# Kernel optimization log

Hardware: AMD Instinct MI355X
Metric: run time of the kernel (lower is better)

Reference implementation:

```python
import jax, jax.numpy as jnp
import numpy as np

B, S, H, L = 64, 512, 1024, 5  # batch, seq_len, BiLSTM feature dim (2*512), num fine P labels


def setup_inputs() -> dict:
    key = jax.random.key(0)
    ks = jax.random.split(key, 8)
    feats = jax.random.normal(ks[0], (B, S, H), dtype=jnp.float32)
    labels = jax.random.randint(ks[1], (B, S), 0, L)
    mask = jnp.ones((B, S), dtype=bool)  # CRF requires mask[:, 0] all on
    W_tag = jax.random.normal(ks[2], (H, L), dtype=jnp.float32) * 0.02
    b_tag = jnp.zeros((L,), dtype=jnp.float32)
    start_trans = jax.random.normal(ks[3], (L,), dtype=jnp.float32) * 0.1
    end_trans = jax.random.normal(ks[4], (L,), dtype=jnp.float32) * 0.1
    trans = jax.random.normal(ks[5], (L, L), dtype=jnp.float32) * 0.1
    weights = jax.random.uniform(ks[6], (L,), dtype=jnp.float32, minval=0.5, maxval=1.5)
    return dict(feats=feats, labels=labels, mask=mask, W_tag=W_tag, b_tag=b_tag,
                start_trans=start_trans, end_trans=end_trans, trans=trans, weights=weights)


def reference(feats, labels, mask, W_tag, b_tag, start_trans, end_trans, trans, weights):
    # hidden2tag + relu (as in the torch module: probablity = F.relu(self.hidden2tag(...)))
    emissions = jax.nn.relu(feats @ W_tag + b_tag)  # [B, S, L]
    maskf = mask.astype(emissions.dtype)            # [B, S]

    # ---- weighted CRF negative log-likelihood, reduction='token_mean' ----
    # numerator: gold-path score, per-token emission contributions scaled by class weights
    em_tag = jnp.take_along_axis(emissions, labels[..., None], axis=2)[..., 0]  # [B, S]
    numerator = (start_trans[labels[:, 0]]
                 + jnp.sum(weights[labels] * em_tag * maskf, axis=1)
                 + jnp.sum(trans[labels[:, :-1], labels[:, 1:]] * maskf[:, 1:], axis=1)
                 + end_trans[labels[:, -1]])  # [B]

    # partition function via forward algorithm (scan over time)
    emis_t = emissions[:, 1:].swapaxes(0, 1)  # [S-1, B, L]
    mask_t = mask[:, 1:].T                    # [S-1, B]

    def fwd_step(alpha, x):
        e, m = x  # [B, L], [B]
        new = jax.nn.logsumexp(alpha[:, :, None] + trans[None, :, :], axis=1) + e
        return jnp.where(m[:, None], new, alpha), None

    alpha0 = start_trans[None, :] + emissions[:, 0]  # [B, L]
    alpha, _ = jax.lax.scan(fwd_step, alpha0, (emis_t, mask_t))
    log_z = jax.nn.logsumexp(alpha + end_trans[None, :], axis=1)  # [B]

    loss = -jnp.sum(numerator - log_z) / maskf.sum()

    # ---- Viterbi decode ----
    def vit_step(v, x):
        e, m = x
        scores = v[:, :, None] + trans[None, :, :]  # [B, L_prev, L_cur]
        best = jnp.max(scores, axis=1) + e
        idx = jnp.argmax(scores, axis=1)            # backpointers [B, L]
        return jnp.where(m[:, None], best, v), idx

    v, hist = jax.lax.scan(vit_step, start_trans[None, :] + emissions[:, 0], (emis_t, mask_t))
    last = jnp.argmax(v + end_trans[None, :], axis=1)  # [B] tag at position S-1
    b_idx = jnp.arange(labels.shape[0])

    def back_step(tag, bp):
        prev = bp[b_idx, tag]
        return prev, tag  # emit tag at position t+1

    first, path_rest = jax.lax.scan(back_step, last, hist, reverse=True)  # [B], [S-1, B]
    paths = jnp.concatenate([first[None, :], path_rest], axis=0).T  # [B, S]

    return loss, paths
```

## Files before the change

kernel.cpp:

```cpp
#include <hip/hip_runtime.h>

namespace {

constexpr int kB = 64, kS = 512, kH = 1024, kL = 5;
constexpr int kRows = kB * kS;
constexpr float kNegInf = -1e30f;

__device__ inline float rl(float x, int i) {
  return __uint_as_float(__builtin_amdgcn_readlane(__float_as_uint(x), i));
}

__global__ __launch_bounds__(256) void emis_kernel(
    const float* __restrict__ feats, const float* __restrict__ W,
    const float* __restrict__ b_tag, float* __restrict__ emis,
    float* __restrict__ out_loss, int nwaves) {
  if (blockIdx.x == 0 && threadIdx.x == 0) out_loss[0] = 0.0f;

  const int lane = threadIdx.x & 63;
  const int wave = blockIdx.x * (blockDim.x >> 6) + (threadIdx.x >> 6);

  float wreg[4][20];
#pragma unroll
  for (int k0 = 0; k0 < 4; ++k0) {
    const float4* wp =
        reinterpret_cast<const float4*>(W + (k0 * 256 + lane * 4) * kL);
#pragma unroll
    for (int q = 0; q < 5; ++q) {
      float4 w = wp[q];
      wreg[k0][q * 4 + 0] = w.x;
      wreg[k0][q * 4 + 1] = w.y;
      wreg[k0][q * 4 + 2] = w.z;
      wreg[k0][q * 4 + 3] = w.w;
    }
  }

  for (int row = wave; row < kRows; row += nwaves) {
    const float4* f4 = reinterpret_cast<const float4*>(feats + (size_t)row * kH);
    float acc[kL] = {0.f, 0.f, 0.f, 0.f, 0.f};
#pragma unroll
    for (int k0 = 0; k0 < 4; ++k0) {
      float4 f = f4[(k0 << 6) + lane];
      const float* wr = wreg[k0];
#pragma unroll
      for (int l = 0; l < kL; ++l) {
        acc[l] = fmaf(f.x, wr[l], acc[l]);
        acc[l] = fmaf(f.y, wr[5 + l], acc[l]);
        acc[l] = fmaf(f.z, wr[10 + l], acc[l]);
        acc[l] = fmaf(f.w, wr[15 + l], acc[l]);
      }
    }
#pragma unroll
    for (int off = 32; off >= 1; off >>= 1)
#pragma unroll
      for (int l = 0; l < kL; ++l) acc[l] += __shfl_xor(acc[l], off, 64);
    if (lane < kL)
      emis[(size_t)row * kL + lane] = fmaxf(acc[lane] + b_tag[lane], 0.0f);
  }
}

__global__ __launch_bounds__(1024) void scan_kernel(
    const float* __restrict__ emis, const int* __restrict__ labels,
    const float* __restrict__ start_trans, const float* __restrict__ end_trans,
    const float* __restrict__ trans, const float* __restrict__ weights,
    float* __restrict__ out_loss, float* __restrict__ out_paths) {
  const int b = blockIdx.x;
  const int tid = threadIdx.x;
  const int lane = tid & 63;
  const int wv = tid >> 6;

  __shared__ float e_lds[(kS + 4) * kL];
  __shared__ float v_lds[kS * kL];
  __shared__ float t_lds[25];
  __shared__ unsigned short f_a[kS], f_b[kS];
  __shared__ float M_lds[8 * 25];
  __shared__ double num_sh;
  __shared__ int last_sh;

  {
    const float4* src = reinterpret_cast<const float4*>(emis + (size_t)b * kS * kL);
    float4* dst = reinterpret_cast<float4*>(e_lds);
    for (int i = tid; i < kS * kL / 4; i += 1024) dst[i] = src[i];
    if (tid < 4 * kL) e_lds[kS * kL + tid] = 0.0f;
    if (tid < 25) t_lds[tid] = trans[tid];
  }
  __syncthreads();

  const int j = (lane < kL) ? lane : 0;

  if (wv == 0) {
    const bool act = lane < kL;
    float tf[kL];
#pragma unroll
    for (int i = 0; i < kL; ++i) tf[i] = t_lds[i * kL + j];
    float vd = start_trans[j] + e_lds[j];
    if (act) v_lds[lane] = vd;
    float e0 = e_lds[1 * kL + j], e1 = e_lds[2 * kL + j],
          e2 = e_lds[3 * kL + j], e3 = e_lds[4 * kL + j];
#pragma unroll 4
    for (int t = 1; t < kS; ++t) {
      float en = e_lds[(t + 4) * kL + j];
      float s0 = rl(vd, 0), s1 = rl(vd, 1), s2 = rl(vd, 2), s3 = rl(vd, 3),
            s4 = rl(vd, 4);
      float c0 = s0 + tf[0], c1 = s1 + tf[1], c2 = s2 + tf[2],
            c3 = s3 + tf[3], c4 = s4 + tf[4];
      float m = fmaxf(fmaxf(fmaxf(c0, c1), fmaxf(c2, c3)), c4);
      vd = m + e0;
      if (act) v_lds[t * kL + lane] = vd;
      e0 = e1; e1 = e2; e2 = e3; e3 = en;
    }
    float v0 = rl(vd, 0), v1 = rl(vd, 1), v2 = rl(vd, 2), v3 = rl(vd, 3),
          v4 = rl(vd, 4);
    if (lane == 0) {
      float best = v0 + end_trans[0];
      int last = 0;
      float cc;
      cc = v1 + end_trans[1]; if (cc > best) { best = cc; last = 1; }
      cc = v2 + end_trans[2]; if (cc > best) { best = cc; last = 2; }
      cc = v3 + end_trans[3]; if (cc > best) { best = cc; last = 3; }
      cc = v4 + end_trans[4]; if (cc > best) { best = cc; last = 4; }
      last_sh = last;
    }
  } else if (wv == 1) {
    double num = 0.0;
    for (int t = lane; t < kS; t += 64) {
      int lt = labels[b * kS + t];
      num += (double)weights[lt] * (double)e_lds[t * kL + lt];
      if (t > 0) {
        int lp = labels[b * kS + t - 1];
        num += (double)t_lds[lp * kL + lt];
      }
    }
#pragma unroll
    for (int off = 32; off >= 1; off >>= 1) num += __shfl_xor(num, off, 64);
    if (lane == 0) {
      int l0 = labels[b * kS];
      int lS = labels[b * kS + kS - 1];
      num_sh = num + (double)start_trans[l0] + (double)end_trans[lS];
    }
  } else if (wv < 10) {
    const int c = wv - 2;
    const int t0 = 1 + 64 * c;
    const int t1 = (t0 + 64 < kS) ? (t0 + 64) : kS;
    const int ci = (lane < 25) ? (lane / 5) : 0;
    const int cj = (lane < 25) ? (lane % 5) : 0;
    float tf[kL];
#pragma unroll
    for (int k = 0; k < kL; ++k) tf[k] = t_lds[k * kL + cj];
    float m = (lane < 25 && ci == cj) ? 0.0f : kNegInf;
    float e_cur = e_lds[t0 * kL + cj];
    for (int t = t0; t < t1; ++t) {
      float e_nxt = (t + 1 < t1) ? e_lds[(t + 1) * kL + cj] : 0.0f;
      float m0 = __shfl(m, ci * 5 + 0, 64), m1 = __shfl(m, ci * 5 + 1, 64),
            m2 = __shfl(m, ci * 5 + 2, 64), m3 = __shfl(m, ci * 5 + 3, 64),
            m4 = __shfl(m, ci * 5 + 4, 64);
      float c0 = m0 + tf[0], c1 = m1 + tf[1], c2 = m2 + tf[2],
            c3 = m3 + tf[3], c4 = m4 + tf[4];
      float mx = fmaxf(fmaxf(fmaxf(c0, c1), fmaxf(c2, c3)), c4);
      float s = __expf(c0 - mx) + __expf(c1 - mx) + __expf(c2 - mx) +
                __expf(c3 - mx) + __expf(c4 - mx);
      m = mx + __logf(s) + e_cur;
      e_cur = e_nxt;
    }
    if (lane < 25) M_lds[c * 25 + lane] = m;
  }
  __syncthreads();

  if (tid < kS - 1) {
    float v0 = v_lds[tid * kL + 0], v1 = v_lds[tid * kL + 1],
          v2 = v_lds[tid * kL + 2], v3 = v_lds[tid * kL + 3],
          v4 = v_lds[tid * kL + 4];
    unsigned int w = 0;
#pragma unroll
    for (int q = 0; q < kL; ++q) {
      float best = v0 + t_lds[0 * kL + q];
      int bi = 0;
      float bb;
      bb = v1 + t_lds[1 * kL + q]; if (bb > best) { best = bb; bi = 1; }
      bb = v2 + t_lds[2 * kL + q]; if (bb > best) { best = bb; bi = 2; }
      bb = v3 + t_lds[3 * kL + q]; if (bb > best) { best = bb; bi = 3; }
      bb = v4 + t_lds[4 * kL + q]; if (bb > best) { best = bb; bi = 4; }
      w |= (unsigned int)bi << (3 * q);
    }
    f_a[tid + 1] = (unsigned short)w;
  }
  __syncthreads();

  unsigned short* src = f_a;
  unsigned short* dst = f_b;
  for (int off = 1; off < kS; off <<= 1) {
    if (tid >= 1 && tid < kS) {
      unsigned short v = src[tid];
      if (tid + off < kS) {
        unsigned int a = v, g = src[tid + off], r = 0;
#pragma unroll
        for (int x = 0; x < kL; ++x) {
          unsigned int bx = (g >> (3 * x)) & 7u;
          r |= ((a >> (3 * bx)) & 7u) << (3 * x);
        }
        v = (unsigned short)r;
      }
      dst[tid] = v;
    }
    __syncthreads();
    unsigned short* tmp = src; src = dst; dst = tmp;
  }

  const int last = last_sh;
  if (tid < kS - 1) {
    unsigned short g = src[tid + 1];
    out_paths[(size_t)b * kS + tid] = (float)((g >> (3 * last)) & 7u);
  } else if (tid == kS - 1) {
    out_paths[(size_t)b * kS + tid] = (float)last;
  }

  if (wv == 1) {
    float alpha = start_trans[j] + e_lds[j];
#pragma unroll 1
    for (int c = 0; c < 8; ++c) {
      float a0 = __shfl(alpha, 0, 64), a1 = __shfl(alpha, 1, 64),
            a2 = __shfl(alpha, 2, 64), a3 = __shfl(alpha, 3, 64),
            a4 = __shfl(alpha, 4, 64);
      float c0 = a0 + M_lds[c * 25 + 0 + j], c1 = a1 + M_lds[c * 25 + 5 + j],
            c2 = a2 + M_lds[c * 25 + 10 + j], c3 = a3 + M_lds[c * 25 + 15 + j],
            c4 = a4 + M_lds[c * 25 + 20 + j];
      float mx = fmaxf(fmaxf(fmaxf(c0, c1), fmaxf(c2, c3)), c4);
      float s = __expf(c0 - mx) + __expf(c1 - mx) + __expf(c2 - mx) +
                __expf(c3 - mx) + __expf(c4 - mx);
      alpha = mx + __logf(s);
    }
    float aj[kL];
#pragma unroll
    for (int i = 0; i < kL; ++i) aj[i] = __shfl(alpha, i, 64);
    if (lane == 0) {
      float c0 = aj[0] + end_trans[0], c1 = aj[1] + end_trans[1],
            c2 = aj[2] + end_trans[2], c3 = aj[3] + end_trans[3],
            c4 = aj[4] + end_trans[4];
      float mx = fmaxf(fmaxf(fmaxf(c0, c1), fmaxf(c2, c3)), c4);
      float logz =
          mx + __logf(__expf(c0 - mx) + __expf(c1 - mx) + __expf(c2 - mx) +
                      __expf(c3 - mx) + __expf(c4 - mx));
      double term = num_sh - (double)logz;
      atomicAdd(out_loss, (float)(-term / (double)(kB * kS)));
    }
  }
}

}

extern "C" void kernel_launch(void* const* d_in, const int* in_sizes, int n_in,
                              void* d_out, int out_size, void* d_ws,
                              size_t ws_size, hipStream_t stream) {
  const float* feats = (const float*)d_in[0];
  const int* labels = (const int*)d_in[1];
  const float* W_tag = (const float*)d_in[3];
  const float* b_tag = (const float*)d_in[4];
  const float* start_trans = (const float*)d_in[5];
  const float* end_trans = (const float*)d_in[6];
  const float* trans = (const float*)d_in[7];
  const float* weights = (const float*)d_in[8];

  float* emis = (float*)d_ws;
  float* out = (float*)d_out;

  const int blocks = 1024;
  const int nwaves = blocks * 4;
  emis_kernel<<<blocks, 256, 0, stream>>>(feats, W_tag, b_tag, emis, out,
                                          nwaves);
  scan_kernel<<<kB, 1024, 0, stream>>>(emis, labels, start_trans, end_trans,
                                       trans, weights, out, out + 1);
}
```

Baseline: 233.1 us.

## Process two rows per wave in emissions and shrink CRF scan block to 512

The emission GEMV now has each wave process two feature rows per iteration, doubling the grid to 2048 blocks. The goal is more memory-level parallelism and loads in flight per wave. The CRF scan kernel drops from 1024 to 512 threads and splits the forward-algorithm transfer-matrix work into 6 chunks of 86 steps instead of 8 chunks of 64, with the backpointer pointer-doubling loop adjusted to match. The smaller block may schedule more cheaply, but each chunk's serial scan is longer.

```diff
diff --git a/kernel.cpp b/kernel.cpp
--- a/kernel.cpp
+++ b/kernel.cpp
@@ -5,6 +5,7 @@
 constexpr int kB = 64, kS = 512, kH = 1024, kL = 5;
 constexpr int kRows = kB * kS;
 constexpr float kNegInf = -1e30f;
+constexpr int kChunks = 6;
 
 __device__ inline float rl(float x, int i) {
   return __uint_as_float(__builtin_amdgcn_readlane(__float_as_uint(x), i));
@@ -34,31 +35,44 @@
     }
   }
 
-  for (int row = wave; row < kRows; row += nwaves) {
-    const float4* f4 = reinterpret_cast<const float4*>(feats + (size_t)row * kH);
-    float acc[kL] = {0.f, 0.f, 0.f, 0.f, 0.f};
+  for (int r = 2 * wave; r < kRows; r += 2 * nwaves) {
+    const float4* fa = reinterpret_cast<const float4*>(feats + (size_t)r * kH);
+    const float4* fb =
+        reinterpret_cast<const float4*>(feats + (size_t)(r + 1) * kH);
+    float accA[kL] = {0.f, 0.f, 0.f, 0.f, 0.f};
+    float accB[kL] = {0.f, 0.f, 0.f, 0.f, 0.f};
 #pragma unroll
     for (int k0 = 0; k0 < 4; ++k0) {
-      float4 f = f4[(k0 << 6) + lane];
+      float4 xa = fa[(k0 << 6) + lane];
+      float4 xb = fb[(k0 << 6) + lane];
       const float* wr = wreg[k0];
 #pragma unroll
       for (int l = 0; l < kL; ++l) {
-        acc[l] = fmaf(f.x, wr[l], acc[l]);
-        acc[l] = fmaf(f.y, wr[5 + l], acc[l]);
-        acc[l] = fmaf(f.z, wr[10 + l], acc[l]);
-        acc[l] = fmaf(f.w, wr[15 + l], acc[l]);
+        accA[l] = fmaf(xa.x, wr[l], accA[l]);
+        accA[l] = fmaf(xa.y, wr[5 + l], accA[l]);
+        accA[l] = fmaf(xa.z, wr[10 + l], accA[l]);
+        accA[l] = fmaf(xa.w, wr[15 + l], accA[l]);
+        accB[l] = fmaf(xb.x, wr[l], accB[l]);
+        accB[l] = fmaf(xb.y, wr[5 + l], accB[l]);
+        accB[l] = fmaf(xb.z, wr[10 + l], accB[l]);
+        accB[l] = fmaf(xb.w, wr[15 + l], accB[l]);
       }
     }
 #pragma unroll
     for (int off = 32; off >= 1; off >>= 1)
 #pragma unroll
-      for (int l = 0; l < kL; ++l) acc[l] += __shfl_xor(acc[l], off, 64);
-    if (lane < kL)
-      emis[(size_t)row * kL + lane] = fmaxf(acc[lane] + b_tag[lane], 0.0f);
-  }
-}
-
-__global__ __launch_bounds__(1024) void scan_kernel(
+      for (int l = 0; l < kL; ++l) {
+        accA[l] += __shfl_xor(accA[l], off, 64);
+        accB[l] += __shfl_xor(accB[l], off, 64);
+      }
+    if (lane < kL) {
+      emis[(size_t)r * kL + lane] = fmaxf(accA[lane] + b_tag[lane], 0.0f);
+      emis[(size_t)(r + 1) * kL + lane] = fmaxf(accB[lane] + b_tag[lane], 0.0f);
+    }
+  }
+}
+
+__global__ __launch_bounds__(512) void scan_kernel(
     const float* __restrict__ emis, const int* __restrict__ labels,
     const float* __restrict__ start_trans, const float* __restrict__ end_trans,
     const float* __restrict__ trans, const float* __restrict__ weights,
@@ -72,14 +86,15 @@
   __shared__ float v_lds[kS * kL];
   __shared__ float t_lds[25];
   __shared__ unsigned short f_a[kS], f_b[kS];
-  __shared__ float M_lds[8 * 25];
+  __shared__ float M_lds[kChunks * 25];
   __shared__ double num_sh;
   __shared__ int last_sh;
 
   {
-    const float4* src = reinterpret_cast<const float4*>(emis + (size_t)b * kS * kL);
+    const float4* src =
+        reinterpret_cast<const float4*>(emis + (size_t)b * kS * kL);
     float4* dst = reinterpret_cast<float4*>(e_lds);
-    for (int i = tid; i < kS * kL / 4; i += 1024) dst[i] = src[i];
+    for (int i = tid; i < kS * kL / 4; i += 512) dst[i] = src[i];
     if (tid < 4 * kL) e_lds[kS * kL + tid] = 0.0f;
     if (tid < 25) t_lds[tid] = trans[tid];
   }
@@ -137,10 +152,10 @@
       int lS = labels[b * kS + kS - 1];
       num_sh = num + (double)start_trans[l0] + (double)end_trans[lS];
     }
-  } else if (wv < 10) {
+  } else {
     const int c = wv - 2;
-    const int t0 = 1 + 64 * c;
-    const int t1 = (t0 + 64 < kS) ? (t0 + 64) : kS;
+    const int t0 = 1 + 86 * c;
+    const int t1 = (t0 + 86 < kS) ? (t0 + 86) : kS;
     const int ci = (lane < 25) ? (lane / 5) : 0;
     const int cj = (lane < 25) ? (lane % 5) : 0;
     float tf[kL];
@@ -188,7 +203,7 @@
   unsigned short* src = f_a;
   unsigned short* dst = f_b;
   for (int off = 1; off < kS; off <<= 1) {
-    if (tid >= 1 && tid < kS) {
+    if (tid >= 1) {
       unsigned short v = src[tid];
       if (tid + off < kS) {
         unsigned int a = v, g = src[tid + off], r = 0;
@@ -216,7 +231,7 @@
   if (wv == 1) {
     float alpha = start_trans[j] + e_lds[j];
 #pragma unroll 1
-    for (int c = 0; c < 8; ++c) {
+    for (int c = 0; c < kChunks; ++c) {
       float a0 = __shfl(alpha, 0, 64), a1 = __shfl(alpha, 1, 64),
             a2 = __shfl(alpha, 2, 64), a3 = __shfl(alpha, 3, 64),
             a4 = __shfl(alpha, 4, 64);
@@ -262,10 +277,10 @@
   float* emis = (float*)d_ws;
   float* out = (float*)d_out;
 
-  const int blocks = 1024;
+  const int blocks = 2048;
   const int nwaves = blocks * 4;
   emis_kernel<<<blocks, 256, 0, stream>>>(feats, W_tag, b_tag, emis, out,
                                           nwaves);
-  scan_kernel<<<kB, 1024, 0, stream>>>(emis, labels, start_trans, end_trans,
-                                       trans, weights, out, out + 1);
-}
+  scan_kernel<<<kB, 512, 0, stream>>>(emis, labels, start_trans, end_trans,
+                                      trans, weights, out, out + 1);
+}
```

Result: no change. 234.3 us (+0.5%).
